# Optimization experiments

Measured on AMD Instinct MI355X. Metric: run time of the kernel, lower is better.

## Reference

```python
import jax, jax.numpy as jnp
import numpy as np

NUM_HEADS = 8
EMBED_DIM = 512
EXPAND = 3
RPE_DIM = 512
RPE_LAYERS = 3
B, N = 4, 2048
D1 = (EXPAND * EMBED_DIM) // NUM_HEADS * NUM_HEADS  # 1536
HEAD_DIM = D1 // NUM_HEADS  # 192


def srms(x):
    # SimpleRMSNorm: x / (||x||_2 * d^{-1/2} + eps)
    d = x.shape[-1]
    rms = jnp.linalg.norm(x, axis=-1, keepdims=True) * (d ** -0.5)
    return x / (rms + 1e-8)


def rpe_net(idx, Wp, bp, Wl, bl, Wr, br):
    # idx: (m, 1) relative positions -> (m, h*head_dim)
    h = idx @ Wp.T + bp
    for i in range(Wl.shape[0]):  # fixed small layer count
        h = jax.nn.relu(srms(h)) @ Wl[i].T + bl[i]
    return jax.nn.relu(srms(h)) @ Wr.T + br


def setup_inputs() -> dict:
    key = jax.random.key(0)
    ks = jax.random.split(key, 12)
    s = 0.02
    return {
        "x": jax.random.normal(ks[0], (B, N, EMBED_DIM), jnp.float32),
        "Wu": jax.random.normal(ks[1], (D1, EMBED_DIM), jnp.float32) * s,
        "bu": jnp.zeros((D1,), jnp.float32),
        "Wv": jax.random.normal(ks[2], (D1, EMBED_DIM), jnp.float32) * s,
        "bv": jnp.zeros((D1,), jnp.float32),
        "Wo": jax.random.normal(ks[3], (EMBED_DIM, D1), jnp.float32) * s,
        "bo": jnp.zeros((EMBED_DIM,), jnp.float32),
        "Wp": jax.random.normal(ks[4], (RPE_DIM, 1), jnp.float32) * s,
        "bp": jax.random.normal(ks[5], (RPE_DIM,), jnp.float32) * s,
        "Wl": jax.random.normal(ks[6], (RPE_LAYERS, RPE_DIM, RPE_DIM), jnp.float32) * s,
        "bl": jax.random.normal(ks[7], (RPE_LAYERS, RPE_DIM), jnp.float32) * s,
        "Wr": jax.random.normal(ks[8], (NUM_HEADS * HEAD_DIM, RPE_DIM), jnp.float32) * s,
        "br": jax.random.normal(ks[9], (NUM_HEADS * HEAD_DIM,), jnp.float32) * s,
    }


def reference(x, Wu, bu, Wv, bv, Wo, bo, Wp, bp, Wl, bl, Wr, br):
    b, n, e = x.shape
    d1 = Wu.shape[0]
    hd = d1 // NUM_HEADS
    u = jax.nn.silu(x @ Wu.T + bu)                       # (b, n, d1)
    v = jax.nn.silu(x @ Wv.T + bv)                       # (b, n, d1)
    v = v.reshape(b, n, NUM_HEADS, hd).transpose(0, 2, 1, 3)  # (b, h, n, d)
    # Tno non-causal, par_type=1: indices [0, 1..n-1, 0, -(n-1)..-1]
    pos = jnp.arange(1, n, dtype=x.dtype)
    zero = jnp.zeros((1,), x.dtype)
    idx = jnp.concatenate([zero, pos, zero, -pos[::-1]])[:, None]  # (2n, 1)
    a = rpe_net(idx, Wp, bp, Wl, bl, Wr, br)             # (2n, h*d)
    a = a.reshape(2 * n, NUM_HEADS, hd).transpose(1, 0, 2)  # (h, 2n, d)
    m = 2 * n
    # circular conv of length 2n along sequence, truncate to n
    y = jnp.fft.rfft(v, m, axis=2) * jnp.fft.rfft(a, m, axis=1)[None]
    out = jnp.fft.irfft(y, m, axis=2)[:, :, :n, :]       # (b, h, n, d)
    out = out.transpose(0, 2, 1, 3).reshape(b, n, d1)    # (b, n, d1)
    return (u * out) @ Wo.T + bo
```

## Files before the change

### kernel.cpp

```cpp
#include <hip/hip_runtime.h>

#define N_SEQ 2048
#define M_FFT 4096
#define D1    1536
#define NH    8
#define HD    192
#define ED    512

typedef __bf16 bf16;
typedef __bf16 bf16x2 __attribute__((ext_vector_type(2)));
typedef __bf16 bf16x4 __attribute__((ext_vector_type(4)));
typedef __bf16 bf16x8 __attribute__((ext_vector_type(8)));
typedef float  floatx4 __attribute__((ext_vector_type(4)));

enum { MODE_PLAIN = 0, MODE_SILU_UV = 1, MODE_AT = 3 };

__device__ __forceinline__ void gload16(const void* g, void* l) {
    __builtin_amdgcn_global_load_lds(
        (const __attribute__((address_space(1))) void*)g,
        (__attribute__((address_space(3))) void*)l, 16, 0, 0);
}

template<int MODE, typename OutT>
__global__ __launch_bounds__(256) void gemm_bf16(
    const bf16* __restrict__ A, const bf16* __restrict__ Bw,
    const float* __restrict__ bias, const float* __restrict__ bias2,
    OutT* __restrict__ C, OutT* __restrict__ C2,
    int M, int Nc, int K)
{
    __shared__ __align__(16) bf16 As[128 * 32];
    __shared__ __align__(16) bf16 Bs[128 * 32];

    const int tid  = threadIdx.x;
    const int row0 = blockIdx.y * 128;
    const int col0 = blockIdx.x * 128;
    const int wid  = tid >> 6;
    const int lane = tid & 63;
    const int lm   = lane & 15;
    const int lk   = lane >> 4;
    const int wm   = wid >> 1;
    const int wn   = wid & 1;
    const int ldrow  = tid >> 2;
    const int ldcol8 = (tid & 3) * 8;

    floatx4 acc[4][4] = {};

    const bf16* Ag = A  + ((size_t)(row0 + ldrow)) * K + ldcol8;
    const bf16* Bg = Bw + ((size_t)(col0 + ldrow)) * K + ldcol8;
    bf16* AsW = As + (wid * 16) * 32;
    bf16* BsW = Bs + (wid * 16) * 32;

    for (int k0 = 0; k0 < K; k0 += 32) {
        gload16(Ag + k0, AsW);
        gload16(Ag + (size_t)64 * K + k0, AsW + 64 * 32);
        gload16(Bg + k0, BsW);
        gload16(Bg + (size_t)64 * K + k0, BsW + 64 * 32);
        __syncthreads();

        bf16x8 af[4], bfr[4];
        #pragma unroll
        for (int mi = 0; mi < 4; ++mi)
            af[mi] = *(const bf16x8*)&As[(wm * 64 + mi * 16 + lm) * 32 + lk * 8];
        #pragma unroll
        for (int nj = 0; nj < 4; ++nj)
            bfr[nj] = *(const bf16x8*)&Bs[(wn * 64 + nj * 16 + lm) * 32 + lk * 8];
        #pragma unroll
        for (int mi = 0; mi < 4; ++mi)
            #pragma unroll
            for (int nj = 0; nj < 4; ++nj)
                acc[mi][nj] = __builtin_amdgcn_mfma_f32_16x16x32_bf16(
                    af[mi], bfr[nj], acc[mi][nj], 0, 0, 0);
        __syncthreads();
    }

    const float* bs = bias;
    OutT* dst = C;
    int cadj = 0;
    if (MODE == MODE_SILU_UV && col0 >= D1) { bs = bias2; dst = C2; cadj = D1; }

    float bcol[4];
    #pragma unroll
    for (int nj = 0; nj < 4; ++nj)
        bcol[nj] = bs[col0 - cadj + wn * 64 + nj * 16 + lm];

    #pragma unroll
    for (int mi = 0; mi < 4; ++mi) {
        const int rbase = row0 + wm * 64 + mi * 16 + lk * 4;
        #pragma unroll
        for (int nj = 0; nj < 4; ++nj) {
            const int col = col0 - cadj + wn * 64 + nj * 16 + lm;
            float vals[4];
            #pragma unroll
            for (int r = 0; r < 4; ++r) {
                float val = acc[mi][nj][r] + bcol[nj];
                if (MODE == MODE_SILU_UV)
                    val = val / (1.0f + __expf(-val));
                vals[r] = val;
            }
            if (MODE == MODE_SILU_UV) {
                int b = rbase >> 11, s = rbase & 2047;
                bf16x4 o;
                #pragma unroll
                for (int r = 0; r < 4; ++r) o[r] = (bf16)vals[r];
                *(bf16x4*)&((bf16*)dst)[((size_t)(b * D1 + col)) * N_SEQ + s] = o;
            } else if (MODE == MODE_AT) {
                float4 o = make_float4(vals[0], vals[1], vals[2], vals[3]);
                *(float4*)&((float*)C)[(size_t)col * M + rbase] = o;
            } else {
                #pragma unroll
                for (int r = 0; r < 4; ++r)
                    C[(size_t)(rbase + r) * Nc + col] = (OutT)vals[r];
            }
        }
    }
}

__global__ __launch_bounds__(256) void f2b_kernel(
    const float* __restrict__ in, bf16* __restrict__ out, int n)
{
    int i = (blockIdx.x * 256 + threadIdx.x) * 4;
    if (i >= n) return;
    float4 f = *(const float4*)(in + i);
    union { bf16 h[4]; short4 s; } u4;
    u4.h[0] = (bf16)f.x; u4.h[1] = (bf16)f.y;
    u4.h[2] = (bf16)f.z; u4.h[3] = (bf16)f.w;
    *(short4*)(out + i) = u4.s;
}

__global__ __launch_bounds__(256) void f2b5_kernel(
    const float* __restrict__ s0, const float* __restrict__ s1,
    const float* __restrict__ s2, const float* __restrict__ s3,
    const float* __restrict__ s4, bf16* __restrict__ dst)
{
    const int seg = blockIdx.y;
    const float* src = seg == 0 ? s0 : seg == 1 ? s1 : seg == 2 ? s2
                     : seg == 3 ? s3 : s4;
    int i = (blockIdx.x * 256 + threadIdx.x) * 4;
    float4 f = *(const float4*)(src + i);
    union { bf16 h[4]; short4 s; } u4;
    u4.h[0] = (bf16)f.x; u4.h[1] = (bf16)f.y;
    u4.h[2] = (bf16)f.z; u4.h[3] = (bf16)f.w;
    *(short4*)(dst + (size_t)seg * 786432 + i) = u4.s;
}

__global__ __launch_bounds__(256) void rpe_in_srms_kernel(
    const float* __restrict__ Wp, const float* __restrict__ bp,
    bf16* __restrict__ g)
{
    const int j = blockIdx.x;
    const int tid = threadIdx.x;
    float idxv = (j < N_SEQ) ? (float)j
                             : (j == N_SEQ ? 0.0f : (float)(j - 2 * N_SEQ));
    float h1 = idxv * Wp[tid] + bp[tid];
    float h2 = idxv * Wp[tid + 256] + bp[tid + 256];
    float ss = h1 * h1 + h2 * h2;
    #pragma unroll
    for (int off = 32; off > 0; off >>= 1) ss += __shfl_down(ss, off, 64);
    __shared__ float red[4];
    if ((tid & 63) == 0) red[tid >> 6] = ss;
    __syncthreads();
    float tot = red[0] + red[1] + red[2] + red[3];
    float scale = 1.0f / (sqrtf(tot) * 0.04419417382415922f + 1e-8f);
    g[(size_t)j * ED + tid]       = (bf16)fmaxf(h1 * scale, 0.0f);
    g[(size_t)j * ED + tid + 256] = (bf16)fmaxf(h2 * scale, 0.0f);
}

__global__ __launch_bounds__(256) void srms_relu_kernel(
    const float* __restrict__ in, bf16* __restrict__ out)
{
    const int row = blockIdx.x;
    const int tid = threadIdx.x;
    const float* p = in + (size_t)row * ED;

    float ss = 0.0f;
    for (int i = tid; i < ED; i += 256) { float x = p[i]; ss += x * x; }
    #pragma unroll
    for (int off = 32; off > 0; off >>= 1) ss += __shfl_down(ss, off, 64);
    __shared__ float red[4];
    if ((tid & 63) == 0) red[tid >> 6] = ss;
    __syncthreads();
    float tot = red[0] + red[1] + red[2] + red[3];
    float scale = 1.0f / (sqrtf(tot) * 0.04419417382415922f + 1e-8f);
    for (int i = tid; i < ED; i += 256)
        out[(size_t)row * ED + i] = (bf16)fmaxf(p[i] * scale, 0.0f);
}

#define FFT_LDS_SZ 4381
#define CC1 0.9238795325112867f
#define SS1 0.3826834323650898f
#define RR2 0.7071067811865476f

__device__ __forceinline__ int fpad(int i) { return i + (i >> 4) + 2 * (i >> 8); }

__device__ __forceinline__ float2 cmul(float2 a, float2 b) {
    return make_float2(a.x * b.x - a.y * b.y, a.x * b.y + a.y * b.x);
}
__device__ __forceinline__ float2 cadd(float2 a, float2 b) {
    return make_float2(a.x + b.x, a.y + b.y);
}
__device__ __forceinline__ float2 csub(float2 a, float2 b) {
    return make_float2(a.x - b.x, a.y - b.y);
}
__device__ __forceinline__ float2 cneg_i(float2 a) { return make_float2(a.y, -a.x); }
__device__ __forceinline__ float2 cpos_i(float2 a) { return make_float2(-a.y, a.x); }
__host__ __device__ constexpr int brev4(int t) {
    return ((t & 1) << 3) | ((t & 2) << 1) | ((t & 4) >> 1) | ((t & 8) >> 3);
}

template<bool HZ>
__device__ __forceinline__ void fft16_dif_r4(float2 x[16]) {
    const float2 W1 = make_float2( CC1, -SS1);
    const float2 W2 = make_float2( RR2, -RR2);
    const float2 W3 = make_float2( SS1, -CC1);
    const float2 W6 = make_float2(-RR2, -RR2);
    const float2 W9 = make_float2(-CC1,  SS1);
    #pragma unroll
    for (int n = 0; n < 4; ++n) {
        float2 A, B, C, D;
        if (HZ) { A = x[n]; C = x[n]; B = x[n + 4]; D = x[n + 4]; }
        else {
            A = cadd(x[n], x[n + 8]);  C = csub(x[n], x[n + 8]);
            B = cadd(x[n + 4], x[n + 12]); D = csub(x[n + 4], x[n + 12]);
        }
        float2 s = csub(A, B);
        float2 nid = cneg_i(D);
        float2 m = cadd(C, nid);
        float2 p = csub(C, nid);
        x[n] = cadd(A, B);
        if (n == 0)      { x[4] = s;            x[8]  = m;           x[12] = p; }
        else if (n == 1) { x[5] = cmul(s, W2);  x[9]  = cmul(m, W1); x[13] = cmul(p, W3); }
        else if (n == 2) { x[6] = cneg_i(s);    x[10] = cmul(m, W2); x[14] = cmul(p, W6); }
        else             { x[7] = cmul(s, W6);  x[11] = cmul(m, W3); x[15] = cmul(p, W9); }
    }
    #pragma unroll
    for (int q = 0; q < 16; q += 4) {
        float2 a = x[q], b = x[q + 1], c = x[q + 2], d = x[q + 3];
        float2 a1 = cadd(a, c), c1 = csub(a, c);
        float2 b1 = cadd(b, d), d1 = cneg_i(csub(b, d));
        x[q]     = cadd(a1, b1);
        x[q + 1] = csub(a1, b1);
        x[q + 2] = cadd(c1, d1);
        x[q + 3] = csub(c1, d1);
    }
}

template<bool HALF_OUT>
__device__ __forceinline__ void fft16_dit_inv_r4(float2 x[16]) {
    const float2 V1 = make_float2( CC1, SS1);
    const float2 V2 = make_float2( RR2, RR2);
    const float2 V3 = make_float2( SS1, CC1);
    const float2 V6 = make_float2(-RR2, RR2);
    #pragma unroll
    for (int q = 0; q < 16; q += 4) {
        float2 a = x[q], b = x[q + 1], c = x[q + 2], d = x[q + 3];
        float2 a1 = cadd(a, b), b1 = csub(a, b);
        float2 c1 = cadd(c, d), d1 = csub(c, d);
        float2 t = cpos_i(d1);
        x[q]     = cadd(a1, c1);
        x[q + 2] = csub(a1, c1);
        x[q + 1] = cadd(b1, t);
        x[q + 3] = csub(b1, t);
    }
    #pragma unroll
    for (int n = 0; n < 4; ++n) {
        float2 t1, t2;
        if (n == 0)      { t1 = x[4];             t2 = x[12]; }
        else if (n == 1) { t1 = cmul(x[5],  V2);  t2 = cmul(x[13], V2); }
        else if (n == 2) { t1 = cpos_i(x[6]);     t2 = cpos_i(x[14]); }
        else             { t1 = cmul(x[7],  V6);  t2 = cmul(x[15], V6); }
        float2 P = cadd(x[n], t1), Q = csub(x[n], t1);
        float2 R = cadd(x[n + 8], t2), S = csub(x[n + 8], t2);
        float2 t, u;
        if (n == 0)      { t = R;            u = S; }
        else if (n == 1) { t = cmul(R, V1);  u = cmul(S, V1); }
        else if (n == 2) { t = cmul(R, V2);  u = cmul(S, V2); }
        else             { t = cmul(R, V3);  u = cmul(S, V3); }
        float2 iu = cpos_i(u);
        x[n]     = cadd(P, t);
        x[n + 4] = cadd(Q, iu);
        if (!HALF_OUT) {
            x[n + 8]  = csub(P, t);
            x[n + 12] = csub(Q, iu);
        }
    }
}

__device__ __forceinline__ void build_twl(float2* twl, int tid)
{
    for (int k = tid; k < 2048; k += 256) {
        float sn, cs;
        __sincosf(-6.283185307179586f * (float)k * (1.0f / 4096.0f), &sn, &cs);
        twl[k] = make_float2(cs, sn);
    }
}

template<bool CONJ>
__device__ __forceinline__ void stage_twiddle_tab(
    float2 v[16], const float2* __restrict__ twl, int j, int mult)
{
    #pragma unroll
    for (int tau = 1; tau < 16; ++tau) {
        int m = j * tau * mult;
        float2 t = twl[m & 2047];
        float sg = (m & 2048) ? -1.0f : 1.0f;
        t.x *= sg;
        t.y = CONJ ? -t.y * sg : t.y * sg;
        v[brev4(tau)] = cmul(v[brev4(tau)], t);
    }
}

template<bool HALF_ZERO>
__device__ void fft4096_fwd(float2* d, const float2* twl, int tid)
{
    float2 v[16];
    {
        const int j = tid;
        if (HALF_ZERO) {
            #pragma unroll
            for (int t = 0; t < 8; ++t) v[t] = d[fpad(j + (t << 8))];
            fft16_dif_r4<true>(v);
        } else {
            #pragma unroll
            for (int t = 0; t < 16; ++t) v[t] = d[fpad(j + (t << 8))];
            fft16_dif_r4<false>(v);
        }
        stage_twiddle_tab<false>(v, twl, j, 1);
        #pragma unroll
        for (int p = 0; p < 16; ++p) d[fpad(j + (p << 8))] = v[p];
    }
    __syncthreads();
    {
        const int base = ((tid >> 4) << 8) + (tid & 15);
        #pragma unroll
        for (int t = 0; t < 16; ++t) v[t] = d[fpad(base + (t << 4))];
        fft16_dif_r4<false>(v);
        stage_twiddle_tab<false>(v, twl, tid & 15, 16);
        #pragma unroll
        for (int p = 0; p < 16; ++p) d[fpad(base + (p << 4))] = v[p];
    }
    __syncthreads();
    {
        const int base = tid << 4;
        #pragma unroll
        for (int t = 0; t < 16; ++t) v[t] = d[fpad(base + t)];
        fft16_dif_r4<false>(v);
        #pragma unroll
        for (int p = 0; p < 16; ++p) d[fpad(base + p)] = v[p];
    }
    __syncthreads();
}

template<bool HALF_OUT>
__device__ void fft4096_inv(float2* d, const float2* twl, int tid)
{
    float2 v[16];
    {
        const int base = tid << 4;
        #pragma unroll
        for (int p = 0; p < 16; ++p) v[p] = d[fpad(base + p)];
        fft16_dit_inv_r4<false>(v);
        #pragma unroll
        for (int t = 0; t < 16; ++t) d[fpad(base + t)] = v[t];
    }
    __syncthreads();
    {
        const int base = ((tid >> 4) << 8) + (tid & 15);
        #pragma unroll
        for (int p = 0; p < 16; ++p) v[p] = d[fpad(base + (p << 4))];
        stage_twiddle_tab<true>(v, twl, tid & 15, 16);
        fft16_dit_inv_r4<false>(v);
        #pragma unroll
        for (int t = 0; t < 16; ++t) d[fpad(base + (t << 4))] = v[t];
    }
    __syncthreads();
    {
        const int j = tid;
        #pragma unroll
        for (int p = 0; p < 16; ++p) v[p] = d[fpad(j + (p << 8))];
        stage_twiddle_tab<true>(v, twl, j, 1);
        fft16_dit_inv_r4<HALF_OUT>(v);
        #pragma unroll
        for (int t = 0; t < (HALF_OUT ? 8 : 16); ++t) d[fpad(j + (t << 8))] = v[t];
    }
    __syncthreads();
}

__global__ __launch_bounds__(256) void fft_a_kernel(
    const float* __restrict__ a_t, float2* __restrict__ Wspec)
{
    __shared__ float2 data[FFT_LDS_SZ];
    __shared__ float2 twl[2048];
    const int tid = threadIdx.x;
    const int h = blockIdx.x / 96, dp = blockIdx.x % 96;

    const float* r0 = a_t + ((size_t)(h * HD + 2 * dp)) * M_FFT;
    const float* r1 = r0 + M_FFT;

    build_twl(twl, tid);
    for (int j = tid; j < 4096; j += 256) data[fpad(j)] = make_float2(r0[j], r1[j]);
    __syncthreads();
    fft4096_fwd<false>(data, twl, tid);

    float2* outrow = Wspec + (size_t)blockIdx.x * 4096;
    for (int j = tid; j < 4096; j += 256) outrow[j] = data[fpad(j)];
}

__global__ __launch_bounds__(256) void fft_conv_kernel(
    const bf16* __restrict__ v_t, const float2* __restrict__ Wspec,
    const bf16* __restrict__ u_t, bf16* __restrict__ gated_t)
{
    __shared__ float2 data[FFT_LDS_SZ];
    __shared__ float2 twl[2048];
    const int tid = threadIdx.x;
    const int bx = blockIdx.x;
    const int b  = bx / 768;
    const int r  = bx % 768;
    const int h  = r / 96, dp = r % 96;
    const int ch = h * HD + 2 * dp;

    const bf16* z0 = v_t + ((size_t)(b * D1 + ch)) * N_SEQ;
    const bf16* z1 = z0 + N_SEQ;

    build_twl(twl, tid);
    {
        const int s = tid * 8;
        bf16x8 a0 = *(const bf16x8*)(z0 + s);
        bf16x8 a1 = *(const bf16x8*)(z1 + s);
        #pragma unroll
        for (int i = 0; i < 8; ++i)
            data[fpad(s + i)] = make_float2((float)a0[i], (float)a1[i]);
    }
    __syncthreads();

    fft4096_fwd<true>(data, twl, tid);

    const float2* Wrow = Wspec + (size_t)r * 4096;
    for (int k = tid; k <= 2048; k += 256) {
        int km = (4096 - k) & 4095;
        int p1 = __brev((unsigned)k)  >> 20;
        int p2 = __brev((unsigned)km) >> 20;
        float2 Zk = data[fpad(p1)], Zm = data[fpad(p2)];
        float2 Wk = Wrow[p1], Wm = Wrow[p2];
        float2 V0 = make_float2(0.5f * (Zk.x + Zm.x), 0.5f * (Zk.y - Zm.y));
        float2 V1 = make_float2(0.5f * (Zk.y + Zm.y), 0.5f * (Zm.x - Zk.x));
        float2 A0 = make_float2(0.5f * (Wk.x + Wm.x), 0.5f * (Wk.y - Wm.y));
        float2 A1 = make_float2(0.5f * (Wk.y + Wm.y), 0.5f * (Wm.x - Wk.x));
        float2 P = make_float2(V0.x * A0.x - V0.y * A0.y, V0.x * A0.y + V0.y * A0.x);
        float2 Q = make_float2(V1.x * A1.x - V1.y * A1.y, V1.x * A1.y + V1.y * A1.x);
        data[fpad(p1)] = make_float2(P.x - Q.y, P.y + Q.x);
        if (k != 0 && k != 2048)
            data[fpad(p2)] = make_float2(P.x + Q.y, Q.x - P.y);
    }
    __syncthreads();

    fft4096_inv<true>(data, twl, tid);

    const float inv_m = 1.0f / 4096.0f;
    const bf16* u0 = u_t + ((size_t)(b * D1 + ch)) * N_SEQ;
    const bf16* u1 = u0 + N_SEQ;
    bf16* g0 = gated_t + ((size_t)(b * D1 + ch)) * N_SEQ;
    bf16* g1 = g0 + N_SEQ;
    {
        const int t = tid * 8;
        bf16x8 ua = *(const bf16x8*)(u0 + t);
        bf16x8 ub = *(const bf16x8*)(u1 + t);
        bf16x8 oa, ob;
        #pragma unroll
        for (int i = 0; i < 8; ++i) {
            float2 y = data[fpad(t + i)];
            oa[i] = (bf16)(y.x * inv_m * (float)ua[i]);
            ob[i] = (bf16)(y.y * inv_m * (float)ub[i]);
        }
        *(bf16x8*)(g0 + t) = oa;
        *(bf16x8*)(g1 + t) = ob;
    }
}

__global__ __launch_bounds__(256) void transpose_cs_kernel(
    const bf16* __restrict__ in, bf16* __restrict__ outp)
{
    __shared__ bf16 tile[64 * 68];
    const int c0 = blockIdx.x * 64;
    const int m0 = blockIdx.y * 64;
    const int b  = m0 >> 11;
    const int s0 = m0 & 2047;
    const int tid = threadIdx.x;
    const int cl = tid >> 4;
    const int sc = (tid & 15) * 4;
    #pragma unroll
    for (int p = 0; p < 4; ++p) {
        int c = p * 16 + cl;
        bf16x4 v = *(const bf16x4*)&in[((size_t)(b * D1 + c0 + c)) * N_SEQ + s0 + sc];
        *(bf16x4*)&tile[c * 68 + sc] = v;
    }
    __syncthreads();
    const int sl = tid >> 4;
    const int cc = (tid & 15) * 4;
    #pragma unroll
    for (int p = 0; p < 4; ++p) {
        int s = p * 16 + sl;
        bf16x4 o;
        #pragma unroll
        for (int j = 0; j < 4; ++j) o[j] = tile[(cc + j) * 68 + s];
        *(bf16x4*)&outp[((size_t)(m0 + s)) * D1 + c0 + cc] = o;
    }
}

extern "C" void kernel_launch(void* const* d_in, const int* in_sizes, int n_in,
                              void* d_out, int out_size, void* d_ws, size_t ws_size,
                              hipStream_t stream)
{
    const float* x  = (const float*)d_in[0];
    const float* Wu = (const float*)d_in[1];
    const float* bu = (const float*)d_in[2];
    const float* Wv = (const float*)d_in[3];
    const float* bv = (const float*)d_in[4];
    const float* Wo = (const float*)d_in[5];
    const float* bo = (const float*)d_in[6];
    const float* Wp = (const float*)d_in[7];
    const float* bp = (const float*)d_in[8];
    const float* Wl = (const float*)d_in[9];
    const float* bl = (const float*)d_in[10];
    const float* Wr = (const float*)d_in[11];
    const float* br = (const float*)d_in[12];
    float* out = (float*)d_out;

    float* ws      = (float*)d_ws;
    float* a_t     = ws;
    float* Wspec   = a_t   + 6291456;
    float* h0      = Wspec + 6291456;
    bf16*  bfws    = (bf16*)(h0 + 2097152);
    bf16*  x_bf    = bfws;
    bf16*  w_bf    = x_bf    + 4194304;
    bf16*  Wuv_bf  = w_bf;
    bf16*  Wo_bf   = w_bf    + 2 * 786432;
    bf16*  Wl_bf   = Wo_bf   + 786432;
    bf16*  Wr_bf   = Wl_bf   + 786432;
    bf16*  g_bf    = Wr_bf   + 786432;
    bf16*  u_t     = g_bf    + 2097152;
    bf16*  v_t     = u_t     + 12582912;
    bf16*  gated_t = v_t     + 12582912;
    bf16*  gated   = gated_t + 12582912;

    dim3 blk(256);

    f2b_kernel<<<4194304 / 1024, blk, 0, stream>>>(x, x_bf, 4194304);
    f2b5_kernel<<<dim3(786432 / 1024, 5), blk, 0, stream>>>(
        Wu, Wv, Wo, Wl, Wr, w_bf);

    gemm_bf16<MODE_SILU_UV, bf16><<<dim3(24, 64), blk, 0, stream>>>(
        x_bf, Wuv_bf, bu, bv, u_t, v_t, 8192, 2 * D1, ED);

    rpe_in_srms_kernel<<<4096, blk, 0, stream>>>(Wp, bp, g_bf);
    for (int i = 0; i < 3; ++i) {
        gemm_bf16<MODE_PLAIN, float><<<dim3(4, 32), blk, 0, stream>>>(
            g_bf, Wl_bf + (size_t)i * ED * ED, bl + (size_t)i * ED, nullptr,
            h0, nullptr, 4096, ED, ED);
        srms_relu_kernel<<<4096, blk, 0, stream>>>(h0, g_bf);
    }
    gemm_bf16<MODE_AT, float><<<dim3(12, 32), blk, 0, stream>>>(
        g_bf, Wr_bf, br, nullptr, a_t, nullptr, 4096, D1, ED);

    fft_a_kernel<<<768, blk, 0, stream>>>(a_t, (float2*)Wspec);
    fft_conv_kernel<<<3072, blk, 0, stream>>>(
        v_t, (const float2*)Wspec, u_t, gated_t);

    transpose_cs_kernel<<<dim3(24, 128), blk, 0, stream>>>(gated_t, gated);

    gemm_bf16<MODE_PLAIN, float><<<dim3(4, 64), blk, 0, stream>>>(
        gated, Wo_bf, bo, nullptr, out, nullptr, 8192, ED, D1);
}
```

Measured before the change: 378.3 us.

## Compute FFT twiddles in registers, fuse spectral multiply into inverse FFT, merge converts

Drops the shared-memory twiddle table and its per-block build. Each stage now makes its twiddles in registers from one sincos and a chain of complex multiplies, which frees LDS and may allow more blocks per CU. The pointwise spectral product is folded into the first inverse-FFT stage so it no longer needs its own LDS round trip and barrier. The two fp32-to-bf16 conversion launches are merged into one. The repeated-multiply twiddles add some rounding error.

```diff
diff --git a/kernel.cpp b/kernel.cpp
--- a/kernel.cpp
+++ b/kernel.cpp
@@ -115,32 +115,31 @@
     }
 }
 
-__global__ __launch_bounds__(256) void f2b_kernel(
-    const float* __restrict__ in, bf16* __restrict__ out, int n)
-{
-    int i = (blockIdx.x * 256 + threadIdx.x) * 4;
-    if (i >= n) return;
-    float4 f = *(const float4*)(in + i);
-    union { bf16 h[4]; short4 s; } u4;
-    u4.h[0] = (bf16)f.x; u4.h[1] = (bf16)f.y;
-    u4.h[2] = (bf16)f.z; u4.h[3] = (bf16)f.w;
-    *(short4*)(out + i) = u4.s;
-}
-
-__global__ __launch_bounds__(256) void f2b5_kernel(
-    const float* __restrict__ s0, const float* __restrict__ s1,
-    const float* __restrict__ s2, const float* __restrict__ s3,
-    const float* __restrict__ s4, bf16* __restrict__ dst)
-{
-    const int seg = blockIdx.y;
-    const float* src = seg == 0 ? s0 : seg == 1 ? s1 : seg == 2 ? s2
-                     : seg == 3 ? s3 : s4;
-    int i = (blockIdx.x * 256 + threadIdx.x) * 4;
+__global__ __launch_bounds__(256) void f2b_all_kernel(
+    const float* __restrict__ x,  const float* __restrict__ s0,
+    const float* __restrict__ s1, const float* __restrict__ s2,
+    const float* __restrict__ s3, const float* __restrict__ s4,
+    bf16* __restrict__ x_bf, bf16* __restrict__ w_bf)
+{
+    const int bid = blockIdx.x;
+    const float* src;
+    bf16* dst;
+    size_t off;
+    if (bid < 4096) {
+        src = x; dst = x_bf; off = (size_t)bid * 1024;
+    } else {
+        int t = bid - 4096;
+        int seg = t / 768;
+        src = seg == 0 ? s0 : seg == 1 ? s1 : seg == 2 ? s2 : seg == 3 ? s3 : s4;
+        dst = w_bf + (size_t)seg * 786432;
+        off = (size_t)(t % 768) * 1024;
+    }
+    size_t i = off + (size_t)threadIdx.x * 4;
     float4 f = *(const float4*)(src + i);
     union { bf16 h[4]; short4 s; } u4;
     u4.h[0] = (bf16)f.x; u4.h[1] = (bf16)f.y;
     u4.h[2] = (bf16)f.z; u4.h[3] = (bf16)f.w;
-    *(short4*)(dst + (size_t)seg * 786432 + i) = u4.s;
+    *(short4*)(dst + i) = u4.s;
 }
 
 __global__ __launch_bounds__(256) void rpe_in_srms_kernel(
@@ -285,32 +284,29 @@
     }
 }
 
-__device__ __forceinline__ void build_twl(float2* twl, int tid)
-{
-    for (int k = tid; k < 2048; k += 256) {
-        float sn, cs;
-        __sincosf(-6.283185307179586f * (float)k * (1.0f / 4096.0f), &sn, &cs);
-        twl[k] = make_float2(cs, sn);
-    }
-}
-
-template<bool CONJ>
-__device__ __forceinline__ void stage_twiddle_tab(
-    float2 v[16], const float2* __restrict__ twl, int j, int mult)
-{
-    #pragma unroll
-    for (int tau = 1; tau < 16; ++tau) {
-        int m = j * tau * mult;
-        float2 t = twl[m & 2047];
-        float sg = (m & 2048) ? -1.0f : 1.0f;
-        t.x *= sg;
-        t.y = CONJ ? -t.y * sg : t.y * sg;
-        v[brev4(tau)] = cmul(v[brev4(tau)], t);
-    }
+__device__ __forceinline__ void stage_twiddle_tree(
+    float2 v[16], int j, float rden, float sgn)
+{
+    float s, c;
+    __sincosf(sgn * 6.283185307179586f * (float)j * rden, &s, &c);
+    float2 w[16];
+    w[1] = make_float2(c, s);
+    w[2] = cmul(w[1], w[1]);
+    w[3] = cmul(w[1], w[2]);
+    w[4] = cmul(w[2], w[2]);
+    w[5] = cmul(w[1], w[4]);
+    w[6] = cmul(w[2], w[4]);
+    w[7] = cmul(w[3], w[4]);
+    w[8] = cmul(w[4], w[4]);
+    #pragma unroll
+    for (int t = 9; t < 16; ++t) w[t] = cmul(w[t - 8], w[8]);
+    #pragma unroll
+    for (int tau = 1; tau < 16; ++tau)
+        v[brev4(tau)] = cmul(v[brev4(tau)], w[tau]);
 }
 
 template<bool HALF_ZERO>
-__device__ void fft4096_fwd(float2* d, const float2* twl, int tid)
+__device__ void fft4096_fwd(float2* d, int tid)
 {
     float2 v[16];
     {
@@ -324,7 +320,7 @@
             for (int t = 0; t < 16; ++t) v[t] = d[fpad(j + (t << 8))];
             fft16_dif_r4<false>(v);
         }
-        stage_twiddle_tab<false>(v, twl, j, 1);
+        stage_twiddle_tree(v, j, 1.0f / 4096.0f, -1.0f);
         #pragma unroll
         for (int p = 0; p < 16; ++p) d[fpad(j + (p << 8))] = v[p];
     }
@@ -334,7 +330,7 @@
         #pragma unroll
         for (int t = 0; t < 16; ++t) v[t] = d[fpad(base + (t << 4))];
         fft16_dif_r4<false>(v);
-        stage_twiddle_tab<false>(v, twl, tid & 15, 16);
+        stage_twiddle_tree(v, tid & 15, 1.0f / 256.0f, -1.0f);
         #pragma unroll
         for (int p = 0; p < 16; ++p) d[fpad(base + (p << 4))] = v[p];
     }
@@ -350,56 +346,19 @@
     __syncthreads();
 }
 
-template<bool HALF_OUT>
-__device__ void fft4096_inv(float2* d, const float2* twl, int tid)
-{
-    float2 v[16];
-    {
-        const int base = tid << 4;
-        #pragma unroll
-        for (int p = 0; p < 16; ++p) v[p] = d[fpad(base + p)];
-        fft16_dit_inv_r4<false>(v);
-        #pragma unroll
-        for (int t = 0; t < 16; ++t) d[fpad(base + t)] = v[t];
-    }
-    __syncthreads();
-    {
-        const int base = ((tid >> 4) << 8) + (tid & 15);
-        #pragma unroll
-        for (int p = 0; p < 16; ++p) v[p] = d[fpad(base + (p << 4))];
-        stage_twiddle_tab<true>(v, twl, tid & 15, 16);
-        fft16_dit_inv_r4<false>(v);
-        #pragma unroll
-        for (int t = 0; t < 16; ++t) d[fpad(base + (t << 4))] = v[t];
-    }
-    __syncthreads();
-    {
-        const int j = tid;
-        #pragma unroll
-        for (int p = 0; p < 16; ++p) v[p] = d[fpad(j + (p << 8))];
-        stage_twiddle_tab<true>(v, twl, j, 1);
-        fft16_dit_inv_r4<HALF_OUT>(v);
-        #pragma unroll
-        for (int t = 0; t < (HALF_OUT ? 8 : 16); ++t) d[fpad(j + (t << 8))] = v[t];
-    }
-    __syncthreads();
-}
-
 __global__ __launch_bounds__(256) void fft_a_kernel(
     const float* __restrict__ a_t, float2* __restrict__ Wspec)
 {
     __shared__ float2 data[FFT_LDS_SZ];
-    __shared__ float2 twl[2048];
     const int tid = threadIdx.x;
     const int h = blockIdx.x / 96, dp = blockIdx.x % 96;
 
     const float* r0 = a_t + ((size_t)(h * HD + 2 * dp)) * M_FFT;
     const float* r1 = r0 + M_FFT;
 
-    build_twl(twl, tid);
     for (int j = tid; j < 4096; j += 256) data[fpad(j)] = make_float2(r0[j], r1[j]);
     __syncthreads();
-    fft4096_fwd<false>(data, twl, tid);
+    fft4096_fwd<false>(data, tid);
 
     float2* outrow = Wspec + (size_t)blockIdx.x * 4096;
     for (int j = tid; j < 4096; j += 256) outrow[j] = data[fpad(j)];
@@ -410,7 +369,6 @@
     const bf16* __restrict__ u_t, bf16* __restrict__ gated_t)
 {
     __shared__ float2 data[FFT_LDS_SZ];
-    __shared__ float2 twl[2048];
     const int tid = threadIdx.x;
     const int bx = blockIdx.x;
     const int b  = bx / 768;
@@ -421,7 +379,6 @@
     const bf16* z0 = v_t + ((size_t)(b * D1 + ch)) * N_SEQ;
     const bf16* z1 = z0 + N_SEQ;
 
-    build_twl(twl, tid);
     {
         const int s = tid * 8;
         bf16x8 a0 = *(const bf16x8*)(z0 + s);
@@ -432,28 +389,55 @@
     }
     __syncthreads();
 
-    fft4096_fwd<true>(data, twl, tid);
+    fft4096_fwd<true>(data, tid);
 
     const float2* Wrow = Wspec + (size_t)r * 4096;
-    for (int k = tid; k <= 2048; k += 256) {
-        int km = (4096 - k) & 4095;
-        int p1 = __brev((unsigned)k)  >> 20;
-        int p2 = __brev((unsigned)km) >> 20;
-        float2 Zk = data[fpad(p1)], Zm = data[fpad(p2)];
-        float2 Wk = Wrow[p1], Wm = Wrow[p2];
-        float2 V0 = make_float2(0.5f * (Zk.x + Zm.x), 0.5f * (Zk.y - Zm.y));
-        float2 V1 = make_float2(0.5f * (Zk.y + Zm.y), 0.5f * (Zm.x - Zk.x));
-        float2 A0 = make_float2(0.5f * (Wk.x + Wm.x), 0.5f * (Wk.y - Wm.y));
-        float2 A1 = make_float2(0.5f * (Wk.y + Wm.y), 0.5f * (Wm.x - Wk.x));
-        float2 P = make_float2(V0.x * A0.x - V0.y * A0.y, V0.x * A0.y + V0.y * A0.x);
-        float2 Q = make_float2(V1.x * A1.x - V1.y * A1.y, V1.x * A1.y + V1.y * A1.x);
-        data[fpad(p1)] = make_float2(P.x - Q.y, P.y + Q.x);
-        if (k != 0 && k != 2048)
-            data[fpad(p2)] = make_float2(P.x + Q.y, Q.x - P.y);
-    }
-    __syncthreads();
-
-    fft4096_inv<true>(data, twl, tid);
+    float2 v[16];
+    {
+        const int base = tid << 4;
+        #pragma unroll
+        for (int i = 0; i < 16; ++i) {
+            const int p  = base + i;
+            const int k  = __brev((unsigned)p) >> 20;
+            const int km = (4096 - k) & 4095;
+            const int p2 = __brev((unsigned)km) >> 20;
+            float2 Zk = data[fpad(p)];
+            float2 Zm = data[fpad(p2)];
+            float2 Wk = Wrow[p];
+            float2 Wm = Wrow[p2];
+            float2 V0 = make_float2(0.5f * (Zk.x + Zm.x), 0.5f * (Zk.y - Zm.y));
+            float2 V1 = make_float2(0.5f * (Zk.y + Zm.y), 0.5f * (Zm.x - Zk.x));
+            float2 A0 = make_float2(0.5f * (Wk.x + Wm.x), 0.5f * (Wk.y - Wm.y));
+            float2 A1 = make_float2(0.5f * (Wk.y + Wm.y), 0.5f * (Wm.x - Wk.x));
+            float2 P = cmul(V0, A0), Q = cmul(V1, A1);
+            v[i] = make_float2(P.x - Q.y, P.y + Q.x);
+        }
+        __syncthreads();
+        fft16_dit_inv_r4<false>(v);
+        #pragma unroll
+        for (int i = 0; i < 16; ++i) data[fpad(base + i)] = v[i];
+    }
+    __syncthreads();
+    {
+        const int base = ((tid >> 4) << 8) + (tid & 15);
+        #pragma unroll
+        for (int p = 0; p < 16; ++p) v[p] = data[fpad(base + (p << 4))];
+        stage_twiddle_tree(v, tid & 15, 1.0f / 256.0f, 1.0f);
+        fft16_dit_inv_r4<false>(v);
+        #pragma unroll
+        for (int t = 0; t < 16; ++t) data[fpad(base + (t << 4))] = v[t];
+    }
+    __syncthreads();
+    {
+        const int j = tid;
+        #pragma unroll
+        for (int p = 0; p < 16; ++p) v[p] = data[fpad(j + (p << 8))];
+        stage_twiddle_tree(v, j, 1.0f / 4096.0f, 1.0f);
+        fft16_dit_inv_r4<true>(v);
+        #pragma unroll
+        for (int t = 0; t < 8; ++t) data[fpad(j + (t << 8))] = v[t];
+    }
+    __syncthreads();
 
     const float inv_m = 1.0f / 4096.0f;
     const bf16* u0 = u_t + ((size_t)(b * D1 + ch)) * N_SEQ;
@@ -544,9 +528,8 @@
 
     dim3 blk(256);
 
-    f2b_kernel<<<4194304 / 1024, blk, 0, stream>>>(x, x_bf, 4194304);
-    f2b5_kernel<<<dim3(786432 / 1024, 5), blk, 0, stream>>>(
-        Wu, Wv, Wo, Wl, Wr, w_bf);
+    f2b_all_kernel<<<4096 + 5 * 768, blk, 0, stream>>>(
+        x, Wu, Wv, Wo, Wl, Wr, x_bf, w_bf);
 
     gemm_bf16<MODE_SILU_UV, bf16><<<dim3(24, 64), blk, 0, stream>>>(
         x_bf, Wuv_bf, bu, bv, u_t, v_t, 8192, 2 * D1, ED);
```

After: 365.5 us. -3.4%, faster.
